# Kernel tuning notes

Hardware: AMD Instinct MI355X
Metric: run time of the kernel (lower is better)

Reference implementation:

```python
import jax, jax.numpy as jnp
import numpy as np

N = 8192        # nodes
E = 262144      # edges (avg degree 32)
IN_CH = 256
CH = 128
SLOPE = 0.2     # PyG GATv2Conv default negative_slope


def gatv2(x, src, dst, wl, wr, att, b):
    """Single-head GATv2Conv (PyG defaults: share_weights=False, self-loops
    already appended to src/dst). x: [N, in]; wl, wr: [out, in]; att: [out]."""
    xl = x @ wl.T                      # [N, out] source-side transform (x_j)
    xr = x @ wr.T                      # [N, out] target-side transform (x_i)
    # per-edge attention logit: att . LeakyReLU(x_l[src] + x_r[dst])
    e = jax.nn.leaky_relu(xl[src] + xr[dst], SLOPE) @ att   # [E']
    # segment softmax over incoming edges of each target node
    m = jax.ops.segment_max(e, dst, num_segments=N)
    p = jnp.exp(e - m[dst])
    s = jax.ops.segment_sum(p, dst, num_segments=N)
    alpha = p / s[dst]                 # every node has a self-loop -> s > 0
    out = jax.ops.segment_sum(alpha[:, None] * xl[src], dst, num_segments=N)
    return out + b


def setup_inputs() -> dict:
    key = jax.random.key(0)
    ks = jax.random.split(key, 2 + 5 * 3)
    inp = {
        "x": jax.random.normal(ks[0], (N, IN_CH), dtype=jnp.float32),
        "edge_index": jax.random.randint(ks[1], (2, E), 0, N, dtype=jnp.int64),
    }
    dims = [(CH, IN_CH), (2 * CH, CH), (CH, 2 * CH), (CH, 2 * CH), (IN_CH, CH)]
    ki = 2
    for i, (oc, ic) in enumerate(dims, start=1):
        sc = (2.0 / (ic + oc)) ** 0.5  # glorot-ish
        inp[f"w{i}l"] = jax.random.normal(ks[ki], (oc, ic), dtype=jnp.float32) * sc
        inp[f"w{i}r"] = jax.random.normal(ks[ki + 1], (oc, ic), dtype=jnp.float32) * sc
        inp[f"a{i}"] = jax.random.normal(ks[ki + 2], (oc,), dtype=jnp.float32) * sc
        inp[f"b{i}"] = jnp.zeros((oc,), dtype=jnp.float32)
        ki += 3
    return inp


def reference(x, edge_index,
              w1l, w1r, a1, b1,
              w2l, w2r, a2, b2,
              w3l, w3r, a3, b3,
              w4l, w4r, a4, b4,
              w5l, w5r, a5, b5):
    loops = jnp.arange(N, dtype=edge_index.dtype)
    src = jnp.concatenate([edge_index[0], loops])   # add_self_loops=True
    dst = jnp.concatenate([edge_index[1], loops])
    h = jax.nn.relu(gatv2(x, src, dst, w1l, w1r, a1, b1))          # [N, CH]
    z = jax.nn.relu(gatv2(h, src, dst, w2l, w2r, a2, b2))          # [N, 2CH]
    re = jax.nn.relu(gatv2(z, src, dst, w3l, w3r, a3, b3))         # [N, CH]
    recon_edge = jax.nn.sigmoid(re @ re.T)                         # [N, N]
    xd = jax.nn.relu(gatv2(z, src, dst, w4l, w4r, a4, b4))         # [N, CH]
    x_rec = jax.nn.relu(gatv2(xd, src, dst, w5l, w5r, a5, b5))     # [N, IN_CH]
    return recon_edge, x_rec, z
```

## Files before the change

kernel.cpp:

```cpp
#include <hip/hip_runtime.h>
#include <hip/hip_bf16.h>
#include <math.h>

#define N_NODES 8192
#define N_EDGES 262144
#define EP (N_EDGES + N_NODES)
#define SLOPE 0.2f

typedef short bf16x8 __attribute__((ext_vector_type(8)));
typedef short short4v __attribute__((ext_vector_type(4)));
typedef unsigned short u16x8 __attribute__((ext_vector_type(8)));
typedef float f32x4 __attribute__((ext_vector_type(4)));

__global__ void extract_hist(const int* __restrict__ raw,
                             int* __restrict__ esrc, int* __restrict__ edst,
                             int* __restrict__ counts) {
    __shared__ int sflag;
    int t = threadIdx.x;
    if (t < 64) {
        unsigned long long b = __ballot(raw[2 * t + 1] != 0);
        if (t == 0) sflag = (b == 0ULL) ? 1 : 0;
    }
    __syncthreads();
    int i64f = sflag;
    int k = blockIdx.x * blockDim.x + t;
    if (k >= N_EDGES) return;
    int s, d;
    if (i64f) {
        s = raw[2 * (size_t)k];
        d = raw[2 * ((size_t)N_EDGES + k)];
    } else {
        s = raw[k];
        d = raw[N_EDGES + k];
    }
    esrc[k] = s;
    edst[k] = d;
    atomicAdd(&counts[d], 1);
}

__global__ void scan_k(const int* __restrict__ counts, int* __restrict__ row_ptr) {
    __shared__ int part[256];
    int t = threadIdx.x;
    int base = t * 32;
    int loc[32];
    int s = 0;
    for (int i = 0; i < 32; ++i) { loc[i] = s; s += counts[base + i] + 1; }
    part[t] = s;
    __syncthreads();
    for (int off = 1; off < 256; off <<= 1) {
        int tmp = (t >= off) ? part[t - off] : 0;
        __syncthreads();
        part[t] += tmp;
        __syncthreads();
    }
    int incl = part[t];
    int excl = incl - s;
    for (int i = 0; i < 32; ++i) row_ptr[base + i] = excl + loc[i];
    if (t == 255) row_ptr[N_NODES] = incl;
}

__global__ void scatter_k(const int* __restrict__ esrc, const int* __restrict__ edst,
                          const int* __restrict__ row_ptr, int* __restrict__ cursor,
                          int* __restrict__ ssrc) {
    int k = blockIdx.x * blockDim.x + threadIdx.x;
    if (k >= EP) return;
    int s, d;
    if (k < N_EDGES) { s = esrc[k]; d = edst[k]; }
    else             { s = d = k - N_EDGES; }
    int pos = row_ptr[d] + atomicAdd(&cursor[d], 1);
    ssrc[pos] = s;
}

struct WPrep {
    const float* wl[5];
    const float* wr[5];
    int oc[5];
    int lk[5];
};

__global__ void prep_all(WPrep P, const float* __restrict__ x,
                         short* __restrict__ W3all, short* __restrict__ A3) {
    int gid = blockIdx.x * blockDim.x + threadIdx.x;
    if (gid < 524288) {
        int r = gid >> 6;
        int c4 = (gid & 63) << 2;
        f32x4 a = *(const f32x4*)&x[((size_t)r << 8) + c4];
        short4v h4, l4;
#pragma unroll
        for (int j = 0; j < 4; ++j) {
            __hip_bfloat16 hb = __float2bfloat16(a[j]);
            float hf = __bfloat162float(hb);
            __hip_bfloat16 lb = __float2bfloat16(a[j] - hf);
            h4[j] = *(short*)&hb;
            l4[j] = *(short*)&lb;
        }
        size_t ro = (size_t)r * 768;
        *(short4v*)&A3[ro + c4] = h4;
        *(short4v*)&A3[ro + 256 + c4] = l4;
        *(short4v*)&A3[ro + 512 + c4] = h4;
    } else {
        int g = gid - 524288;
        int l = g >> 16;
        if (l >= 5) return;
        int rem = g & 65535;
        int lk = P.lk[l], K = 1 << lk;
        int r = rem >> lk, c = rem & (K - 1);
        int OC = P.oc[l];
        const float* w = (r < OC) ? P.wl[l] : P.wr[l];
        int rr = (r < OC) ? r : r - OC;
        float a = w[((size_t)rr << lk) + c];
        __hip_bfloat16 hb = __float2bfloat16(a);
        float hf = __bfloat162float(hb);
        __hip_bfloat16 lb = __float2bfloat16(a - hf);
        size_t ro = (size_t)l * 196608 + (size_t)r * 3 * K;
        W3all[ro + c] = *(short*)&hb;
        W3all[ro + K + c] = *(short*)&hb;
        W3all[ro + 2 * K + c] = *(short*)&lb;
    }
}

#if __has_builtin(__builtin_amdgcn_global_load_lds)
#define GL16(gsrc, lbase, lofs)                                                       \
    __builtin_amdgcn_global_load_lds((const __attribute__((address_space(1))) void*)(gsrc), \
                                     (__attribute__((address_space(3))) void*)(lbase), 16, 0, 0)
#else
#define GL16(gsrc, lbase, lofs) (*(bf16x8*)((lbase) + (lofs)) = *(const bf16x8*)(gsrc))
#endif

__global__ __launch_bounds__(256) void gemm_bf16_nt(const short* __restrict__ A3,
                                                    const short* __restrict__ W3,
                                                    unsigned short* __restrict__ XLb,
                                                    float* __restrict__ XRf,
                                                    int K3, int N2, int ocl, int lgpl) {
    __shared__ __align__(16) short As[2][4096];
    __shared__ __align__(16) short Bs[2][4096];
    int tid = threadIdx.x;
    int gx = gridDim.x;
    int lgx = (gx == 8) ? 3 : 2;
    int orig = blockIdx.x + (blockIdx.y << lgx);
    int nwg = gx << 7;
    int swzb = (orig & 7) * (nwg >> 3) + (orig >> 3);
    int bx = swzb & (gx - 1), by = swzb >> lgx;
    int i0 = by * 64, j0 = bx * 64;

    int wave = tid >> 6, lane = tid & 63;
    int b0 = wave * 1024 + lane * 16;
    int row0 = b0 >> 7;
    int rb0 = b0 & 127;
    int scb = rb0 ^ ((row0 & 7) << 4);
    const short* gA0 = A3 + (size_t)(i0 + row0) * K3 + (scb >> 1);
    const short* gA1 = A3 + (size_t)(i0 + row0 + 32) * K3 + (scb >> 1);
    const short* gB0 = W3 + (size_t)(j0 + row0) * K3 + (scb >> 1);
    const short* gB1 = W3 + (size_t)(j0 + row0 + 32) * K3 + (scb >> 1);
    int lofs = lane * 8;

#define STAGE(pb, k0s)                                      \
    do {                                                    \
        GL16(gA0 + (k0s), &As[pb][wave * 512], lofs);       \
        GL16(gA1 + (k0s), &As[pb][2048 + wave * 512], lofs);\
        GL16(gB0 + (k0s), &Bs[pb][wave * 512], lofs);       \
        GL16(gB1 + (k0s), &Bs[pb][2048 + wave * 512], lofs);\
    } while (0)

    int wr = (wave >> 1) * 32, wc = (wave & 1) * 32;
    int lm = lane & 15, quad = lane >> 4;
    f32x4 acc[2][2] = {};
    int nt = K3 >> 6;
    STAGE(0, 0);
    int cur = 0;
    for (int t = 0; t < nt; ++t) {
        if (t + 1 < nt) {
            STAGE(cur ^ 1, (t + 1) << 6);
            asm volatile("s_waitcnt vmcnt(4)" ::: "memory");
        } else {
            asm volatile("s_waitcnt vmcnt(0)" ::: "memory");
        }
        __builtin_amdgcn_s_barrier();
        __builtin_amdgcn_sched_barrier(0);
        const char* Ab = (const char*)&As[cur][0];
        const char* Bb = (const char*)&Bs[cur][0];
#pragma unroll
        for (int ks = 0; ks < 2; ++ks) {
            int kb = ks * 64 + quad * 16;
            bf16x8 a[2], b[2];
#pragma unroll
            for (int u = 0; u < 2; ++u) {
                int r = wr + u * 16 + lm;
                a[u] = *(const bf16x8*)(Ab + (((r << 7) | kb) ^ ((r & 7) << 4)));
            }
#pragma unroll
            for (int v = 0; v < 2; ++v) {
                int r = wc + v * 16 + lm;
                b[v] = *(const bf16x8*)(Bb + (((r << 7) | kb) ^ ((r & 7) << 4)));
            }
#pragma unroll
            for (int u = 0; u < 2; ++u)
#pragma unroll
                for (int v = 0; v < 2; ++v)
                    acc[u][v] = __builtin_amdgcn_mfma_f32_16x16x32_bf16(a[u], b[v], acc[u][v], 0, 0, 0);
        }
        __builtin_amdgcn_sched_barrier(0);
        __builtin_amdgcn_s_barrier();
        cur ^= 1;
    }
#undef STAGE
    int plm = (1 << lgpl) - 1;
#pragma unroll
    for (int u = 0; u < 2; ++u)
#pragma unroll
        for (int v = 0; v < 2; ++v)
#pragma unroll
            for (int r = 0; r < 4; ++r) {
                int row = i0 + wr + u * 16 + quad * 4 + r;
                int col = j0 + wc + v * 16 + lm;
                int slab = col >> lgpl;
                int wn = col & plm;
                float val = acc[u][v][r];
                size_t base = (size_t)slab * N_NODES * ocl + (size_t)row * ocl;
                if (wn < ocl) {
                    __hip_bfloat16 hb = __float2bfloat16(val);
                    XLb[base + wn] = *(unsigned short*)&hb;
                } else {
                    XRf[base + wn - ocl] = val;
                }
            }
}

#define LSTR 136

__global__ __launch_bounds__(256) void recon_sym(const unsigned short* __restrict__ Rb,
                                                 float* __restrict__ C) {
    __shared__ __align__(16) short Sh[2 * 128 * LSTR];
    short* As = Sh;
    short* Bs = Sh + 128 * LSTR;
    int tid = threadIdx.x;
    int orig = blockIdx.x;
    int s = (orig & 7) * 260 + (orig >> 3);
    float ff = 64.5f - sqrtf(64.5f * 64.5f - 2.0f * (float)s);
    int bi = (int)ff;
    while (bi > 0 && 64 * bi - bi * (bi - 1) / 2 > s) --bi;
    while (64 * (bi + 1) - (bi + 1) * bi / 2 <= s) ++bi;
    int bj = bi + (s - (64 * bi - bi * (bi - 1) / 2));
    int i0 = bi * 128, j0 = bj * 128;
    const short* R = (const short*)Rb;
#pragma unroll
    for (int c = 0; c < 8; ++c) {
        int idx = tid + c * 256;
        int row = idx >> 4, col = (idx & 15) * 8;
        *(bf16x8*)(&As[row * LSTR + col]) = *(const bf16x8*)(&R[(size_t)(i0 + row) * 128 + col]);
        *(bf16x8*)(&Bs[row * LSTR + col]) = *(const bf16x8*)(&R[(size_t)(j0 + row) * 128 + col]);
    }
    __syncthreads();
    int wave = tid >> 6, lane = tid & 63;
    int wr = (wave >> 1) * 64, wc = (wave & 1) * 64;
    int lm = lane & 15, quad = lane >> 4;
    f32x4 acc[4][4] = {};
#pragma unroll
    for (int ks = 0; ks < 4; ++ks) {
        int ko = ks * 32 + quad * 8;
        bf16x8 a[4], b[4];
#pragma unroll
        for (int u = 0; u < 4; ++u)
            a[u] = *(const bf16x8*)(&As[(wr + u * 16 + lm) * LSTR + ko]);
#pragma unroll
        for (int v = 0; v < 4; ++v)
            b[v] = *(const bf16x8*)(&Bs[(wc + v * 16 + lm) * LSTR + ko]);
#pragma unroll
        for (int u = 0; u < 4; ++u)
#pragma unroll
            for (int v = 0; v < 4; ++v)
                acc[u][v] = __builtin_amdgcn_mfma_f32_16x16x32_bf16(a[u], b[v], acc[u][v], 0, 0, 0);
    }
#pragma unroll
    for (int u = 0; u < 4; ++u)
#pragma unroll
        for (int v = 0; v < 4; ++v)
#pragma unroll
            for (int r = 0; r < 4; ++r) {
                acc[u][v][r] = 1.0f / (1.0f + __expf(-acc[u][v][r]));
                int row = i0 + wr + u * 16 + quad * 4 + r;
                int col = j0 + wc + v * 16 + lm;
                C[(size_t)row * 8192 + col] = acc[u][v][r];
            }
    if (bi != bj) {
        __syncthreads();
        float* T = (float*)Sh;
#pragma unroll
        for (int u = 0; u < 4; ++u)
#pragma unroll
            for (int v = 0; v < 4; ++v)
#pragma unroll
                for (int r = 0; r < 4; ++r)
                    T[(wr + u * 16 + quad * 4 + r) * 129 + (wc + v * 16 + lm)] = acc[u][v][r];
        __syncthreads();
#pragma unroll
        for (int it = 0; it < 64; ++it) {
            int idx = tid + it * 256;
            int rp = idx >> 7, cp = idx & 127;
            C[(size_t)(j0 + rp) * 8192 + (i0 + cp)] = T[cp * 129 + rp];
        }
    }
}

struct GatP {
    const float* att; const float* bias;
    float* outf; short* a3; unsigned short* rb;
    const unsigned short* xlb; const float* xrf;
};

__device__ __forceinline__ void cvt8(u16x8 w, float* v) {
#pragma unroll
    for (int j = 0; j < 8; ++j) v[j] = __uint_as_float(((unsigned)w[j]) << 16);
}

__global__ __launch_bounds__(256) void gat128(const int* __restrict__ row_ptr,
                                              const int* __restrict__ ssrc,
                                              GatP P0, GatP P1) {
    __shared__ float sacc[16][128];
    __shared__ float ss[16];
    int d = blockIdx.x & (N_NODES - 1);
    GatP P = (blockIdx.x >= N_NODES) ? P1 : P0;
    int t = threadIdx.x, ln = t & 15, g = t >> 4;
    int beg = row_ptr[d], end = row_ptr[d + 1];
    float xr[8], at[8];
    {
        f32x4 a0 = *(const f32x4*)&P.xrf[(size_t)d * 128 + ln * 8];
        f32x4 a1 = *(const f32x4*)&P.xrf[(size_t)d * 128 + ln * 8 + 4];
        f32x4 b0 = *(const f32x4*)&P.att[ln * 8];
        f32x4 b1 = *(const f32x4*)&P.att[ln * 8 + 4];
#pragma unroll
        for (int j = 0; j < 4; ++j) { xr[j] = a0[j]; xr[4 + j] = a1[j]; at[j] = b0[j]; at[4 + j] = b1[j]; }
    }
    float s = 0.0f, acc[8] = {};
    int p = beg + g;
    for (; p + 16 < end; p += 32) {
        int s0 = ssrc[p], s1 = ssrc[p + 16];
        float v0[8], v1[8];
        cvt8(*(const u16x8*)&P.xlb[(size_t)s0 * 128 + ln * 8], v0);
        cvt8(*(const u16x8*)&P.xlb[(size_t)s1 * 128 + ln * 8], v1);
        float e0 = 0.0f, e1 = 0.0f;
#pragma unroll
        for (int j = 0; j < 8; ++j) {
            float u0 = v0[j] + xr[j]; u0 = (u0 > 0.0f) ? u0 : SLOPE * u0; e0 += u0 * at[j];
            float u1 = v1[j] + xr[j]; u1 = (u1 > 0.0f) ? u1 : SLOPE * u1; e1 += u1 * at[j];
        }
#pragma unroll
        for (int off = 8; off; off >>= 1) {
            e0 += __shfl_xor(e0, off, 64);
            e1 += __shfl_xor(e1, off, 64);
        }
        float q0 = __expf(e0), q1 = __expf(e1);
        s += q0 + q1;
#pragma unroll
        for (int j = 0; j < 8; ++j) acc[j] += q0 * v0[j] + q1 * v1[j];
    }
    if (p < end) {
        int si = ssrc[p];
        float v[8];
        cvt8(*(const u16x8*)&P.xlb[(size_t)si * 128 + ln * 8], v);
        float e = 0.0f;
#pragma unroll
        for (int j = 0; j < 8; ++j) {
            float u = v[j] + xr[j];
            u = (u > 0.0f) ? u : SLOPE * u;
            e += u * at[j];
        }
#pragma unroll
        for (int off = 8; off; off >>= 1) e += __shfl_xor(e, off, 64);
        float q = __expf(e);
        s += q;
#pragma unroll
        for (int j = 0; j < 8; ++j) acc[j] += q * v[j];
    }
#pragma unroll
    for (int j = 0; j < 8; ++j) sacc[g][ln * 8 + j] = acc[j];
    if (ln == 0) ss[g] = s;
    __syncthreads();
    if (t < 128) {
        float tot = 0.0f, st = 0.0f;
#pragma unroll
        for (int w = 0; w < 16; ++w) { tot += sacc[w][t]; st += ss[w]; }
        float val = fmaxf(tot / st + P.bias[t], 0.0f);
        if (P.outf) P.outf[(size_t)d * 128 + t] = val;
        if (P.a3) {
            __hip_bfloat16 hb = __float2bfloat16(val);
            float hf = __bfloat162float(hb);
            __hip_bfloat16 lb = __float2bfloat16(val - hf);
            size_t ro = (size_t)d * 384;
            P.a3[ro + t] = *(short*)&hb;
            P.a3[ro + 128 + t] = *(short*)&lb;
            P.a3[ro + 256 + t] = *(short*)&hb;
        }
        if (P.rb) {
            __hip_bfloat16 hb = __float2bfloat16(val);
            P.rb[d * 128 + t] = *(unsigned short*)&hb;
        }
    }
}

__global__ __launch_bounds__(256) void gat256(const int* __restrict__ row_ptr,
                                              const int* __restrict__ ssrc,
                                              const unsigned short* __restrict__ xlb,
                                              const float* __restrict__ xrf,
                                              const float* __restrict__ att,
                                              const float* __restrict__ bias,
                                              float* __restrict__ outf,
                                              short* __restrict__ a3) {
    __shared__ float sacc[8][256];
    __shared__ float ss[8];
    int d = blockIdx.x, t = threadIdx.x;
    int ln = t & 31, g = t >> 5;
    int beg = row_ptr[d], end = row_ptr[d + 1];
    float xr[8], at[8];
    {
        f32x4 a0 = *(const f32x4*)&xrf[(size_t)d * 256 + ln * 8];
        f32x4 a1 = *(const f32x4*)&xrf[(size_t)d * 256 + ln * 8 + 4];
        f32x4 b0 = *(const f32x4*)&att[ln * 8];
        f32x4 b1 = *(const f32x4*)&att[ln * 8 + 4];
#pragma unroll
        for (int j = 0; j < 4; ++j) { xr[j] = a0[j]; xr[4 + j] = a1[j]; at[j] = b0[j]; at[4 + j] = b1[j]; }
    }
    float s = 0.0f, acc[8] = {};
    int p = beg + g;
    for (; p + 8 < end; p += 16) {
        int s0 = ssrc[p], s1 = ssrc[p + 8];
        float v0[8], v1[8];
        cvt8(*(const u16x8*)&xlb[(size_t)s0 * 256 + ln * 8], v0);
        cvt8(*(const u16x8*)&xlb[(size_t)s1 * 256 + ln * 8], v1);
        float e0 = 0.0f, e1 = 0.0f;
#pragma unroll
        for (int j = 0; j < 8; ++j) {
            float u0 = v0[j] + xr[j]; u0 = (u0 > 0.0f) ? u0 : SLOPE * u0; e0 += u0 * at[j];
            float u1 = v1[j] + xr[j]; u1 = (u1 > 0.0f) ? u1 : SLOPE * u1; e1 += u1 * at[j];
        }
#pragma unroll
        for (int off = 16; off; off >>= 1) {
            e0 += __shfl_xor(e0, off, 64);
            e1 += __shfl_xor(e1, off, 64);
        }
        float q0 = __expf(e0), q1 = __expf(e1);
        s += q0 + q1;
#pragma unroll
        for (int j = 0; j < 8; ++j) acc[j] += q0 * v0[j] + q1 * v1[j];
    }
    if (p < end) {
        int si = ssrc[p];
        float v[8];
        cvt8(*(const u16x8*)&xlb[(size_t)si * 256 + ln * 8], v);
        float e = 0.0f;
#pragma unroll
        for (int j = 0; j < 8; ++j) {
            float u = v[j] + xr[j];
            u = (u > 0.0f) ? u : SLOPE * u;
            e += u * at[j];
        }
#pragma unroll
        for (int off = 16; off; off >>= 1) e += __shfl_xor(e, off, 64);
        float q = __expf(e);
        s += q;
#pragma unroll
        for (int j = 0; j < 8; ++j) acc[j] += q * v[j];
    }
#pragma unroll
    for (int j = 0; j < 8; ++j) sacc[g][ln * 8 + j] = acc[j];
    if (ln == 0) ss[g] = s;
    __syncthreads();
    {
        float tot = 0.0f, st = 0.0f;
#pragma unroll
        for (int w = 0; w < 8; ++w) { tot += sacc[w][t]; st += ss[w]; }
        float val = fmaxf(tot / st + bias[t], 0.0f);
        if (outf) outf[(size_t)d * 256 + t] = val;
        if (a3) {
            __hip_bfloat16 hb = __float2bfloat16(val);
            float hf = __bfloat162float(hb);
            __hip_bfloat16 lb = __float2bfloat16(val - hf);
            size_t ro = (size_t)d * 768;
            a3[ro + t] = *(short*)&hb;
            a3[ro + 256 + t] = *(short*)&lb;
            a3[ro + 512 + t] = *(short*)&hb;
        }
    }
}

static inline int ceil_div(int a, int b) { return (a + b - 1) / b; }

extern "C" void kernel_launch(void* const* d_in, const int* in_sizes, int n_in,
                              void* d_out, int out_size, void* d_ws, size_t ws_size,
                              hipStream_t stream) {
    const float* x    = (const float*)d_in[0];
    const int*   eraw = (const int*)d_in[1];

    WPrep P;
    const float* att[5];
    const float* bia[5];
    for (int l = 0; l < 5; ++l) {
        P.wl[l] = (const float*)d_in[2 + 4 * l + 0];
        P.wr[l] = (const float*)d_in[2 + 4 * l + 1];
        att[l]  = (const float*)d_in[2 + 4 * l + 2];
        bia[l]  = (const float*)d_in[2 + 4 * l + 3];
    }
    const int och[5]  = {128, 256, 128, 128, 256};
    const int logK[5] = {8, 7, 8, 8, 7};
    for (int l = 0; l < 5; ++l) { P.oc[l] = och[l]; P.lk[l] = logK[l]; }

    float* outp  = (float*)d_out;
    float* recon = outp;
    float* xrec  = outp + (size_t)67108864;
    float* zout  = outp + (size_t)69206016;

    float* W = (float*)d_ws;
    unsigned short* XLb = (unsigned short*)W;
    float* XRf   = W + 1048576;
    short* A3    = (short*)(W + 3145728);
    short* W3all = (short*)(W + 6291456);
    unsigned short* Rb = (unsigned short*)(W + 6782976);
    int* I       = (int*)(W + 7307264);
    int* counts  = I;
    int* cursor  = I + 8192;
    int* row_ptr = I + 16384;
    int* ssrc    = I + 24577;
    int* esrc    = I + 294913;
    int* edst    = I + 557057;

    hipMemsetAsync(counts, 0, 2 * 8192 * sizeof(int), stream);
    extract_hist<<<ceil_div(N_EDGES, 256), 256, 0, stream>>>(eraw, esrc, edst, counts);
    scan_k<<<1, 256, 0, stream>>>(counts, row_ptr);
    scatter_k<<<ceil_div(EP, 256), 256, 0, stream>>>(esrc, edst, row_ptr, cursor, ssrc);

    prep_all<<<3328, 256, 0, stream>>>(P, x, W3all, A3);

    {
        dim3 g(4, 128);
        gemm_bf16_nt<<<g, 256, 0, stream>>>(A3, W3all + 0 * 196608, XLb, XRf, 768, 256, 128, 8);
        GatP g0{att[0], bia[0], nullptr, A3, nullptr, XLb, XRf};
        gat128<<<N_NODES, 256, 0, stream>>>(row_ptr, ssrc, g0, g0);
    }
    {
        dim3 g(8, 128);
        gemm_bf16_nt<<<g, 256, 0, stream>>>(A3, W3all + 1 * 196608, XLb, XRf, 384, 512, 256, 9);
        gat256<<<N_NODES, 256, 0, stream>>>(row_ptr, ssrc, XLb, XRf, att[1], bia[1], zout, A3);
    }
    {
        dim3 g(8, 128);
        gemm_bf16_nt<<<g, 256, 0, stream>>>(A3, W3all + 2 * 196608, XLb, XRf, 768, 512, 128, 8);
        GatP g2{att[2], bia[2], nullptr, nullptr, Rb, XLb, XRf};
        GatP g3{att[3], bia[3], nullptr, A3, nullptr, XLb + (size_t)N_NODES * 128, XRf + (size_t)N_NODES * 128};
        gat128<<<2 * N_NODES, 256, 0, stream>>>(row_ptr, ssrc, g2, g3);
        recon_sym<<<2080, 256, 0, stream>>>(Rb, recon);
    }
    {
        dim3 g(8, 128);
        gemm_bf16_nt<<<g, 256, 0, stream>>>(A3, W3all + 4 * 196608, XLb, XRf, 384, 512, 256, 9);
        gat256<<<N_NODES, 256, 0, stream>>>(row_ptr, ssrc, XLb, XRf, att[4], bia[4], xrec, nullptr);
    }
}
```

Measured before the change: 521.7 us.

## Fuse prologue kernels, restructure gat256 lanes, use nontemporal recon stores

```diff
diff --git a/kernel.cpp b/kernel.cpp
--- a/kernel.cpp
+++ b/kernel.cpp
@@ -11,65 +11,6 @@
 typedef short short4v __attribute__((ext_vector_type(4)));
 typedef unsigned short u16x8 __attribute__((ext_vector_type(8)));
 typedef float f32x4 __attribute__((ext_vector_type(4)));
-
-__global__ void extract_hist(const int* __restrict__ raw,
-                             int* __restrict__ esrc, int* __restrict__ edst,
-                             int* __restrict__ counts) {
-    __shared__ int sflag;
-    int t = threadIdx.x;
-    if (t < 64) {
-        unsigned long long b = __ballot(raw[2 * t + 1] != 0);
-        if (t == 0) sflag = (b == 0ULL) ? 1 : 0;
-    }
-    __syncthreads();
-    int i64f = sflag;
-    int k = blockIdx.x * blockDim.x + t;
-    if (k >= N_EDGES) return;
-    int s, d;
-    if (i64f) {
-        s = raw[2 * (size_t)k];
-        d = raw[2 * ((size_t)N_EDGES + k)];
-    } else {
-        s = raw[k];
-        d = raw[N_EDGES + k];
-    }
-    esrc[k] = s;
-    edst[k] = d;
-    atomicAdd(&counts[d], 1);
-}
-
-__global__ void scan_k(const int* __restrict__ counts, int* __restrict__ row_ptr) {
-    __shared__ int part[256];
-    int t = threadIdx.x;
-    int base = t * 32;
-    int loc[32];
-    int s = 0;
-    for (int i = 0; i < 32; ++i) { loc[i] = s; s += counts[base + i] + 1; }
-    part[t] = s;
-    __syncthreads();
-    for (int off = 1; off < 256; off <<= 1) {
-        int tmp = (t >= off) ? part[t - off] : 0;
-        __syncthreads();
-        part[t] += tmp;
-        __syncthreads();
-    }
-    int incl = part[t];
-    int excl = incl - s;
-    for (int i = 0; i < 32; ++i) row_ptr[base + i] = excl + loc[i];
-    if (t == 255) row_ptr[N_NODES] = incl;
-}
-
-__global__ void scatter_k(const int* __restrict__ esrc, const int* __restrict__ edst,
-                          const int* __restrict__ row_ptr, int* __restrict__ cursor,
-                          int* __restrict__ ssrc) {
-    int k = blockIdx.x * blockDim.x + threadIdx.x;
-    if (k >= EP) return;
-    int s, d;
-    if (k < N_EDGES) { s = esrc[k]; d = edst[k]; }
-    else             { s = d = k - N_EDGES; }
-    int pos = row_ptr[d] + atomicAdd(&cursor[d], 1);
-    ssrc[pos] = s;
-}
 
 struct WPrep {
     const float* wl[5];
@@ -78,8 +19,10 @@
     int lk[5];
 };
 
-__global__ void prep_all(WPrep P, const float* __restrict__ x,
-                         short* __restrict__ W3all, short* __restrict__ A3) {
+__global__ void prologue(WPrep P, const float* __restrict__ x,
+                         short* __restrict__ W3all, short* __restrict__ A3,
+                         const int* __restrict__ raw, int* __restrict__ counts) {
+    __shared__ int sflag;
     int gid = blockIdx.x * blockDim.x + threadIdx.x;
     if (gid < 524288) {
         int r = gid >> 6;
@@ -98,10 +41,9 @@
         *(short4v*)&A3[ro + c4] = h4;
         *(short4v*)&A3[ro + 256 + c4] = l4;
         *(short4v*)&A3[ro + 512 + c4] = h4;
-    } else {
+    } else if (gid < 851968) {
         int g = gid - 524288;
         int l = g >> 16;
-        if (l >= 5) return;
         int rem = g & 65535;
         int lk = P.lk[l], K = 1 << lk;
         int r = rem >> lk, c = rem & (K - 1);
@@ -116,7 +58,61 @@
         W3all[ro + c] = *(short*)&hb;
         W3all[ro + K + c] = *(short*)&hb;
         W3all[ro + 2 * K + c] = *(short*)&lb;
-    }
+    } else {
+        int t = threadIdx.x;
+        if (t < 64) {
+            unsigned long long b = __ballot(raw[2 * t + 1] != 0);
+            if (t == 0) sflag = (b == 0ULL) ? 1 : 0;
+        }
+        __syncthreads();
+        int k = gid - 851968;
+        int d = sflag ? raw[2 * ((size_t)N_EDGES + k)] : raw[N_EDGES + k];
+        atomicAdd(&counts[d], 1);
+    }
+}
+
+__global__ void scan_k(const int* __restrict__ counts, int* __restrict__ row_ptr) {
+    __shared__ int buf[8192];
+    __shared__ int part[256];
+    int t = threadIdx.x;
+    for (int i = 0; i < 32; ++i) buf[i * 256 + t] = counts[i * 256 + t];
+    __syncthreads();
+    int base = t * 32;
+    int loc[32];
+    int s = 0;
+    for (int i = 0; i < 32; ++i) { loc[i] = s; s += buf[base + i] + 1; }
+    part[t] = s;
+    __syncthreads();
+    for (int off = 1; off < 256; off <<= 1) {
+        int tmp = (t >= off) ? part[t - off] : 0;
+        __syncthreads();
+        part[t] += tmp;
+        __syncthreads();
+    }
+    int incl = part[t];
+    int excl = incl - s;
+    for (int i = 0; i < 32; ++i) row_ptr[base + i] = excl + loc[i];
+    if (t == 255) row_ptr[N_NODES] = incl;
+}
+
+__global__ void scatter_k(const int* __restrict__ raw, const int* __restrict__ row_ptr,
+                          int* __restrict__ cursor, int* __restrict__ ssrc) {
+    __shared__ int sflag;
+    int t = threadIdx.x;
+    if (t < 64) {
+        unsigned long long b = __ballot(raw[2 * t + 1] != 0);
+        if (t == 0) sflag = (b == 0ULL) ? 1 : 0;
+    }
+    __syncthreads();
+    int k = blockIdx.x * blockDim.x + t;
+    if (k >= EP) return;
+    int s, d;
+    if (k < N_EDGES) {
+        if (sflag) { s = raw[2 * (size_t)k]; d = raw[2 * ((size_t)N_EDGES + k)]; }
+        else       { s = raw[k]; d = raw[N_EDGES + k]; }
+    } else s = d = k - N_EDGES;
+    int pos = row_ptr[d] + atomicAdd(&cursor[d], 1);
+    ssrc[pos] = s;
 }
 
 #if __has_builtin(__builtin_amdgcn_global_load_lds)
@@ -127,22 +123,19 @@
 #define GL16(gsrc, lbase, lofs) (*(bf16x8*)((lbase) + (lofs)) = *(const bf16x8*)(gsrc))
 #endif
 
-__global__ __launch_bounds__(256) void gemm_bf16_nt(const short* __restrict__ A3,
-                                                    const short* __restrict__ W3,
-                                                    unsigned short* __restrict__ XLb,
-                                                    float* __restrict__ XRf,
-                                                    int K3, int N2, int ocl, int lgpl) {
-    __shared__ __align__(16) short As[2][4096];
-    __shared__ __align__(16) short Bs[2][4096];
+__global__ __launch_bounds__(256) void gemm_std(const short* __restrict__ A3,
+                                                const short* __restrict__ W3,
+                                                unsigned short* __restrict__ XLb,
+                                                float* __restrict__ XRf,
+                                                int K3, int ocl, int lgpl, int lgx) {
+    __shared__ __align__(16) short SH[16384];
+    int nwg = gridDim.x;
+    int orig = blockIdx.x;
+    int swzb = (orig & 7) * (nwg >> 3) + (orig >> 3);
+    int bx = swzb & ((1 << lgx) - 1), by = swzb >> lgx;
+
     int tid = threadIdx.x;
-    int gx = gridDim.x;
-    int lgx = (gx == 8) ? 3 : 2;
-    int orig = blockIdx.x + (blockIdx.y << lgx);
-    int nwg = gx << 7;
-    int swzb = (orig & 7) * (nwg >> 3) + (orig >> 3);
-    int bx = swzb & (gx - 1), by = swzb >> lgx;
     int i0 = by * 64, j0 = bx * 64;
-
     int wave = tid >> 6, lane = tid & 63;
     int b0 = wave * 1024 + lane * 16;
     int row0 = b0 >> 7;
@@ -156,10 +149,12 @@
 
 #define STAGE(pb, k0s)                                      \
     do {                                                    \
-        GL16(gA0 + (k0s), &As[pb][wave * 512], lofs);       \
-        GL16(gA1 + (k0s), &As[pb][2048 + wave * 512], lofs);\
-        GL16(gB0 + (k0s), &Bs[pb][wave * 512], lofs);       \
-        GL16(gB1 + (k0s), &Bs[pb][2048 + wave * 512], lofs);\
+        short* Ad = SH + (pb) * 4096;                       \
+        short* Bd = SH + 8192 + (pb) * 4096;                \
+        GL16(gA0 + (k0s), Ad + wave * 512, lofs);           \
+        GL16(gA1 + (k0s), Ad + 2048 + wave * 512, lofs);    \
+        GL16(gB0 + (k0s), Bd + wave * 512, lofs);           \
+        GL16(gB1 + (k0s), Bd + 2048 + wave * 512, lofs);    \
     } while (0)
 
     int wr = (wave >> 1) * 32, wc = (wave & 1) * 32;
@@ -177,8 +172,8 @@
         }
         __builtin_amdgcn_s_barrier();
         __builtin_amdgcn_sched_barrier(0);
-        const char* Ab = (const char*)&As[cur][0];
-        const char* Bb = (const char*)&Bs[cur][0];
+        const char* Ab = (const char*)(SH + cur * 4096);
+        const char* Bb = (const char*)(SH + 8192 + cur * 4096);
 #pragma unroll
         for (int ks = 0; ks < 2; ++ks) {
             int kb = ks * 64 + quad * 16;
@@ -238,6 +233,7 @@
     int s = (orig & 7) * 260 + (orig >> 3);
     float ff = 64.5f - sqrtf(64.5f * 64.5f - 2.0f * (float)s);
     int bi = (int)ff;
+    if (bi < 0) bi = 0;
     while (bi > 0 && 64 * bi - bi * (bi - 1) / 2 > s) --bi;
     while (64 * (bi + 1) - (bi + 1) * bi / 2 <= s) ++bi;
     int bj = bi + (s - (64 * bi - bi * (bi - 1) / 2));
@@ -277,10 +273,11 @@
         for (int v = 0; v < 4; ++v)
 #pragma unroll
             for (int r = 0; r < 4; ++r) {
-                acc[u][v][r] = 1.0f / (1.0f + __expf(-acc[u][v][r]));
+                float sg = 1.0f / (1.0f + __expf(-acc[u][v][r]));
+                acc[u][v][r] = sg;
                 int row = i0 + wr + u * 16 + quad * 4 + r;
                 int col = j0 + wc + v * 16 + lm;
-                C[(size_t)row * 8192 + col] = acc[u][v][r];
+                __builtin_nontemporal_store(sg, &C[(size_t)row * 8192 + col]);
             }
     if (bi != bj) {
         __syncthreads();
@@ -297,7 +294,7 @@
         for (int it = 0; it < 64; ++it) {
             int idx = tid + it * 256;
             int rp = idx >> 7, cp = idx & 127;
-            C[(size_t)(j0 + rp) * 8192 + (i0 + cp)] = T[cp * 129 + rp];
+            __builtin_nontemporal_store(T[cp * 129 + rp], &C[(size_t)(j0 + rp) * 8192 + (i0 + cp)]);
         }
     }
 }
@@ -406,69 +403,71 @@
                                               const float* __restrict__ bias,
                                               float* __restrict__ outf,
                                               short* __restrict__ a3) {
-    __shared__ float sacc[8][256];
-    __shared__ float ss[8];
+    __shared__ float sacc[16][256];
+    __shared__ float ss[16];
     int d = blockIdx.x, t = threadIdx.x;
-    int ln = t & 31, g = t >> 5;
+    int ln = t & 15, g = t >> 4;
     int beg = row_ptr[d], end = row_ptr[d + 1];
-    float xr[8], at[8];
-    {
-        f32x4 a0 = *(const f32x4*)&xrf[(size_t)d * 256 + ln * 8];
-        f32x4 a1 = *(const f32x4*)&xrf[(size_t)d * 256 + ln * 8 + 4];
-        f32x4 b0 = *(const f32x4*)&att[ln * 8];
-        f32x4 b1 = *(const f32x4*)&att[ln * 8 + 4];
-#pragma unroll
-        for (int j = 0; j < 4; ++j) { xr[j] = a0[j]; xr[4 + j] = a1[j]; at[j] = b0[j]; at[4 + j] = b1[j]; }
-    }
-    float s = 0.0f, acc[8] = {};
+    float xr[16], at[16];
+#pragma unroll
+    for (int q = 0; q < 4; ++q) {
+        f32x4 a = *(const f32x4*)&xrf[(size_t)d * 256 + ln * 16 + q * 4];
+        f32x4 b = *(const f32x4*)&att[ln * 16 + q * 4];
+#pragma unroll
+        for (int j = 0; j < 4; ++j) { xr[q * 4 + j] = a[j]; at[q * 4 + j] = b[j]; }
+    }
+    float s = 0.0f, acc[16] = {};
     int p = beg + g;
-    for (; p + 8 < end; p += 16) {
-        int s0 = ssrc[p], s1 = ssrc[p + 8];
-        float v0[8], v1[8];
-        cvt8(*(const u16x8*)&xlb[(size_t)s0 * 256 + ln * 8], v0);
-        cvt8(*(const u16x8*)&xlb[(size_t)s1 * 256 + ln * 8], v1);
+    for (; p + 16 < end; p += 32) {
+        int s0 = ssrc[p], s1 = ssrc[p + 16];
+        float v0[16], v1[16];
+        cvt8(*(const u16x8*)&xlb[(size_t)s0 * 256 + ln * 16], v0);
+        cvt8(*(const u16x8*)&xlb[(size_t)s0 * 256 + ln * 16 + 8], v0 + 8);
+        cvt8(*(const u16x8*)&xlb[(size_t)s1 * 256 + ln * 16], v1);
+        cvt8(*(const u16x8*)&xlb[(size_t)s1 * 256 + ln * 16 + 8], v1 + 8);
         float e0 = 0.0f, e1 = 0.0f;
 #pragma unroll
-        for (int j = 0; j < 8; ++j) {
+        for (int j = 0; j < 16; ++j) {
             float u0 = v0[j] + xr[j]; u0 = (u0 > 0.0f) ? u0 : SLOPE * u0; e0 += u0 * at[j];
             float u1 = v1[j] + xr[j]; u1 = (u1 > 0.0f) ? u1 : SLOPE * u1; e1 += u1 * at[j];
         }
 #pragma unroll
-        for (int off = 16; off; off >>= 1) {
+        for (int off = 8; off; off >>= 1) {
             e0 += __shfl_xor(e0, off, 64);
             e1 += __shfl_xor(e1, off, 64);
         }
         float q0 = __expf(e0), q1 = __expf(e1);
         s += q0 + q1;
 #pragma unroll
-        for (int j = 0; j < 8; ++j) acc[j] += q0 * v0[j] + q1 * v1[j];
+        for (int j = 0; j < 16; ++j) acc[j] += q0 * v0[j] + q1 * v1[j];
     }
     if (p < end) {
         int si = ssrc[p];
-        float v[8];
-        cvt8(*(const u16x8*)&xlb[(size_t)si * 256 + ln * 8], v);
+        float v[16];
+        cvt8(*(const u16x8*)&xlb[(size_t)si * 256 + ln * 16], v);
+        cvt8(*(const u16x8*)&xlb[(size_t)si * 256 + ln * 16 + 8], v + 8);
         float e = 0.0f;
 #pragma unroll
-        for (int j = 0; j < 8; ++j) {
+        for (int j = 0; j < 16; ++j) {
             float u = v[j] + xr[j];
             u = (u > 0.0f) ? u : SLOPE * u;
             e += u * at[j];
         }
 #pragma unroll
-        for (int off = 16; off; off >>= 1) e += __shfl_xor(e, off, 64);
+        for (int off = 8; off; off >>= 1) e += __shfl_xor(e, off, 64);
         float q = __expf(e);
         s += q;
 #pragma unroll
-        for (int j = 0; j < 8; ++j) acc[j] += q * v[j];
-    }
-#pragma unroll
-    for (int j = 0; j < 8; ++j) sacc[g][ln * 8 + j] = acc[j];
+        for (int j = 0; j < 16; ++j) acc[j] += q * v[j];
+    }
+#pragma unroll
+    for (int j = 0; j < 16; ++j) sacc[g][ln * 16 + j] = acc[j];
     if (ln == 0) ss[g] = s;
     __syncthreads();
     {
         float tot = 0.0f, st = 0.0f;
 #pragma unroll
-        for (int w = 0; w < 8; ++w) { tot += sacc[w][t]; st += ss[w]; }
+        for (int w = 0; w < 16; ++w) { tot += sacc[w][t]; st += ss[w]; }
         float val = fmaxf(tot / st + bias[t], 0.0f);
         if (outf) outf[(size_t)d * 256 + t] = val;
         if (a3) {
@@ -520,38 +519,30 @@
     int* cursor  = I + 8192;
     int* row_ptr = I + 16384;
     int* ssrc    = I + 24577;
-    int* esrc    = I + 294913;
-    int* edst    = I + 557057;
 
     hipMemsetAsync(counts, 0, 2 * 8192 * sizeof(int), stream);
-    extract_hist<<<ceil_div(N_EDGES, 256), 256, 0, stream>>>(eraw, esrc, edst, counts);
+    prologue<<<4352, 256, 0, stream>>>(P, x, W3all, A3, eraw, counts);
     scan_k<<<1, 256, 0, stream>>>(counts, row_ptr);
-    scatter_k<<<ceil_div(EP, 256), 256, 0, stream>>>(esrc, edst, row_ptr, cursor, ssrc);
-
-    prep_all<<<3328, 256, 0, stream>>>(P, x, W3all, A3);
+    scatter_k<<<ceil_div(EP, 256), 256, 0, stream>>>(eraw, row_ptr, cursor, ssrc);
 
     {
-        dim3 g(4, 128);
-        gemm_bf16_nt<<<g, 256, 0, stream>>>(A3, W3all + 0 * 196608, XLb, XRf, 768, 256, 128, 8);
+        gemm_std<<<512, 256, 0, stream>>>(A3, W3all + 0 * 196608, XLb, XRf, 768, 128, 8, 2);
         GatP g0{att[0], bia[0], nullptr, A3, nullptr, XLb, XRf};
         gat128<<<N_NODES, 256, 0, stream>>>(row_ptr, ssrc, g0, g0);
     }
     {
-        dim3 g(8, 128);
-        gemm_bf16_nt<<<g, 256, 0, stream>>>(A3, W3all + 1 * 196608, XLb, XRf, 384, 512, 256, 9);
+        gemm_std<<<1024, 256, 0, stream>>>(A3, W3all + 1 * 196608, XLb, XRf, 384, 256, 9, 3);
         gat256<<<N_NODES, 256, 0, stream>>>(row_ptr, ssrc, XLb, XRf, att[1], bia[1], zout, A3);
     }
     {
-        dim3 g(8, 128);
-        gemm_bf16_nt<<<g, 256, 0, stream>>>(A3, W3all + 2 * 196608, XLb, XRf, 768, 512, 128, 8);
+        gemm_std<<<1024, 256, 0, stream>>>(A3, W3all + 2 * 196608, XLb, XRf, 768, 128, 8, 3);
         GatP g2{att[2], bia[2], nullptr, nullptr, Rb, XLb, XRf};
         GatP g3{att[3], bia[3], nullptr, A3, nullptr, XLb + (size_t)N_NODES * 128, XRf + (size_t)N_NODES * 128};
         gat128<<<2 * N_NODES, 256, 0, stream>>>(row_ptr, ssrc, g2, g3);
         recon_sym<<<2080, 256, 0, stream>>>(Rb, recon);
     }
     {
-        dim3 g(8, 128);
-        gemm_bf16_nt<<<g, 256, 0, stream>>>(A3, W3all + 4 * 196608, XLb, XRf, 384, 512, 256, 9);
+        gemm_std<<<1024, 256, 0, stream>>>(A3, W3all + 4 * 196608, XLb, XRf, 384, 256, 9, 3);
         gat256<<<N_NODES, 256, 0, stream>>>(row_ptr, ssrc, XLb, XRf, att[4], bia[4], xrec, nullptr);
     }
 }
```

Result: slower. 538.3 us (+3.2%).
